# Kernel optimization log

Hardware: AMD Instinct MI355X
Metric: run time of the kernel (lower is better)

Reference implementation:

```python
import jax, jax.numpy as jnp
import numpy as np
from jax import lax

BITS = 8
STRIDE = 1
PADDING = 1
SCALE = 2.0 ** (BITS - 1)  # fixed-point scale 2^(bits-1)


def setup_inputs() -> dict:
    key = jax.random.key(0)
    k1, k2, k3 = jax.random.split(key, 3)
    x = jax.random.normal(k1, (32, 128, 56, 56), dtype=jnp.float32)
    W = jax.random.normal(k2, (256, 128, 3, 3), dtype=jnp.float32)
    b = jax.random.normal(k3, (256,), dtype=jnp.float32)
    return {"x": x, "W": W, "b": b}


def reference(x, W, b):
    # to_fix_point: round(v * 2^(bits-1)); torch keeps long ints, but all
    # arithmetic in forward promotes back to float, so float round is exact here.
    w_q = jnp.round(W * SCALE)
    b_q = jnp.round(b * SCALE)
    # calConv: out[i,j] = sum(patch * w_q) / 2^(bits-1) + b_q
    # (square 3x3 kernel makes the original's transposed patch indexing a standard conv)
    out = lax.conv_general_dilated(
        x, w_q,
        window_strides=(STRIDE, STRIDE),
        padding=[(PADDING, PADDING), (PADDING, PADDING)],
        dimension_numbers=("NCHW", "OIHW", "NCHW"),
    )
    return out / SCALE + b_q[None, :, None, None]
```

## Files before the change

kernel.cpp:

```cpp
#include <hip/hip_runtime.h>

typedef _Float16 half8 __attribute__((ext_vector_type(8)));
typedef float floatx4 __attribute__((ext_vector_type(4)));

#define IMG   3136
#define PIMG  3364
#define XP_ELEMS (32 * 58 * 58 * 128)
#define WQ_ELEMS (9 * 256 * 128)

#define AS1 __attribute__((address_space(1)))
#define AS3 __attribute__((address_space(3)))

__global__ __launch_bounds__(256) void prep_kernel(const float* __restrict__ x,
                                                   const float* __restrict__ W,
                                                   _Float16* __restrict__ xp,
                                                   _Float16* __restrict__ wq) {
    const int bid = blockIdx.x;
    const int t   = threadIdx.x;
    if (bid >= 1856) {
        int U  = (bid - 1856) * 256 + t;
        int l  = U & 63;
        int ni = (U >> 6) & 3;
        int wf = (U >> 8) & 3;
        int s  = U >> 10;
        int rs = s >> 2, cc = s & 3;
        int k  = wf * 64 + ni * 16 + (l & 15);
        int c0 = cc * 32 + (l >> 4) * 8;
        _Float16* d = wq + (long)U * 8;
        #pragma unroll
        for (int j = 0; j < 8; ++j)
            d[j] = (_Float16)rintf(W[(k * 128 + c0 + j) * 9 + rs] * 128.0f);
        return;
    }
    const int hh = bid % 58;
    const int n  = bid / 58;
    _Float16* rowbase = xp + ((long)(n * 58 + hh) * 58) * 128;

    if (hh == 0 || hh == 57) {
        #pragma unroll
        for (int i = 0; i < 4; ++i) {
            int idx = i * 256 + t;
            if (idx < 928) *(half8*)(rowbase + idx * 8) = (half8)(_Float16)0.0f;
        }
        return;
    }

    __shared__ _Float16 tile[128 * 57];
    const int h = hh - 1;

    #pragma unroll
    for (int p = 0; p < 7; ++p) {
        int idx = p * 256 + t;
        int c   = idx / 14;
        int w4  = (idx % 14) * 4;
        const float4 v = *(const float4*)(x + ((long)(n * 128 + c) * 56 + h) * 56 + w4);
        _Float16* d = tile + c * 57 + w4;
        d[0] = (_Float16)v.x; d[1] = (_Float16)v.y;
        d[2] = (_Float16)v.z; d[3] = (_Float16)v.w;
    }
    __syncthreads();

    #pragma unroll
    for (int p = 0; p < 4; ++p) {
        int idx = p * 256 + t;
        if (idx < 896) {
            int ww = idx >> 4;
            int c0 = (idx & 15) * 8;
            half8 v;
            #pragma unroll
            for (int j = 0; j < 8; ++j) v[j] = tile[(c0 + j) * 57 + ww];
            *(half8*)(rowbase + (ww + 1) * 128 + c0) = v;
        }
    }
    if (t < 32) {
        int ww = (t >> 4) ? 57 : 0;
        int c0 = (t & 15) * 8;
        *(half8*)(rowbase + ww * 128 + c0) = (half8)(_Float16)0.0f;
    }
}

__global__ __launch_bounds__(512, 2) void conv_mfma_kernel(
    const _Float16* __restrict__ xp, const _Float16* __restrict__ wq,
    const float* __restrict__ b, float* __restrict__ out)
{
    __shared__ __align__(16) _Float16 smem[16384];

    const int tid = threadIdx.x;
    const int l   = tid & 63;
    const int wv  = tid >> 6;
    const int wp  = wv & 1;
    const int wf  = wv >> 1;
    int bx  = blockIdx.x;
    bx = (bx & 7) * 49 + (bx >> 3);

    long pbB[2];
    #pragma unroll
    for (int h = 0; h < 2; ++h) {
        const int pix = bx * 256 + h * 128 + wv * 16 + (l >> 2);
        const int n = pix / IMG, hw = pix % IMG;
        pbB[h] = (long)(n * PIMG + (hw / 56) * 58 + (hw % 56)) * 256
               + ((l & 3) ^ ((l >> 3) & 3)) * 16;
    }
    const int kq = ((l >> 4) ^ ((l >> 1) & 3)) * 8;

    floatx4 acc[8][4] = {};

    auto stageB = [&](int s, int pbuf) {
        const int rs = s >> 2;
        const int cc = s & 3;
        const int r  = (rs * 11) >> 5;
        const int s2 = rs - r * 3;
        const long toff = (long)(r * 58 + s2) * 256 + cc * 64;
        const char* xb = (const char*)xp + toff;
        _Float16* dst = smem + pbuf * 8192 + wv * 512;
        __builtin_amdgcn_global_load_lds((AS1 void*)(xb + pbB[0]), (AS3 void*)dst,          16, 0, 0);
        __builtin_amdgcn_global_load_lds((AS1 void*)(xb + pbB[1]), (AS3 void*)(dst + 4096), 16, 0, 0);
    };
    auto loadA = [&](int s, half8 (&ff)[4]) {
        const char* base = (const char*)wq + (long)(s * 16 + wf * 4) * 1024 + l * 16;
        #pragma unroll
        for (int ni = 0; ni < 4; ++ni)
            ff[ni] = *(const half8*)(base + ni * 1024);
    };

    auto body = [&](int s, half8 (&ffC)[4], half8 (&ffN)[4]) {
        const int pb = s & 1;
        if (s < 35) {
            loadA(s + 1, ffN);
            stageB(s + 1, pb ^ 1);
            asm volatile("s_waitcnt vmcnt(6)" ::: "memory");
        } else {
            asm volatile("s_waitcnt vmcnt(0)" ::: "memory");
        }
        asm volatile("s_barrier" ::: "memory");
        const _Float16* Bs = smem + pb * 8192;
        __builtin_amdgcn_s_setprio(1);
        #pragma unroll
        for (int mi = 0; mi < 8; ++mi) {
            const half8 pf = *(const half8*)(Bs + (wp * 128 + mi * 16 + (l & 15)) * 32 + kq);
            #pragma unroll
            for (int ni = 0; ni < 4; ++ni)
                acc[mi][ni] = __builtin_amdgcn_mfma_f32_16x16x32_f16(pf, ffC[ni], acc[mi][ni], 0, 0, 0);
        }
        __builtin_amdgcn_s_setprio(0);
        asm volatile("s_barrier" ::: "memory");
    };

    half8 ffA[4], ffB[4];
    loadA(0, ffA);
    stageB(0, 0);
    for (int sp = 0; sp < 18; ++sp) {
        body(2 * sp,     ffA, ffB);
        body(2 * sp + 1, ffB, ffA);
    }

    #pragma unroll
    for (int mi = 0; mi < 8; ++mi) {
        const int pix = bx * 256 + wp * 128 + mi * 16 + (l >> 4) * 4;
        const int n  = pix / IMG;
        const int pr = pix - n * IMG;
        float* orow = out + (long)n * 256 * IMG + pr;
        #pragma unroll
        for (int ni = 0; ni < 4; ++ni) {
            const int filt = wf * 64 + ni * 16 + (l & 15);
            const float bq = rintf(b[filt] * 128.0f);
            float4 v;
            v.x = acc[mi][ni][0] * (1.0f / 128.0f) + bq;
            v.y = acc[mi][ni][1] * (1.0f / 128.0f) + bq;
            v.z = acc[mi][ni][2] * (1.0f / 128.0f) + bq;
            v.w = acc[mi][ni][3] * (1.0f / 128.0f) + bq;
            *(float4*)(orow + (long)filt * IMG) = v;
        }
    }
}

__global__ void conv_fallback_kernel(const float* __restrict__ x, const float* __restrict__ W,
                                     const float* __restrict__ b, float* __restrict__ out)
{
    __shared__ float wsm[1152];
    const int k = blockIdx.y;
    for (int i = threadIdx.x; i < 1152; i += 256)
        wsm[i] = rintf(W[k * 1152 + i] * 128.0f);
    __syncthreads();
    const int pix = blockIdx.x * 256 + threadIdx.x;
    const int n = pix / IMG, hw = pix % IMG;
    const int h = hw / 56, w = hw % 56;
    float acc = 0.0f;
    for (int c = 0; c < 128; ++c) {
        const float* xr = x + ((n * 128 + c) * 56) * 56;
        const float* wr = wsm + c * 9;
        #pragma unroll
        for (int r = 0; r < 3; ++r) {
            const int hh = h + r - 1;
            if ((unsigned)hh >= 56u) continue;
            #pragma unroll
            for (int s = 0; s < 3; ++s) {
                const int ww = w + s - 1;
                if ((unsigned)ww >= 56u) continue;
                acc += xr[hh * 56 + ww] * wr[r * 3 + s];
            }
        }
    }
    out[((long)n * 256 + k) * IMG + hw] = acc * (1.0f / 128.0f) + rintf(b[k] * 128.0f);
}

extern "C" void kernel_launch(void* const* d_in, const int* in_sizes, int n_in,
                              void* d_out, int out_size, void* d_ws, size_t ws_size,
                              hipStream_t stream) {
    const float* x = (const float*)d_in[0];
    const float* W = (const float*)d_in[1];
    const float* b = (const float*)d_in[2];
    float* out = (float*)d_out;

    const size_t need = (size_t)XP_ELEMS * 2 + (size_t)WQ_ELEMS * 2;
    if (ws_size >= need) {
        _Float16* xp = (_Float16*)d_ws;
        _Float16* wq = xp + XP_ELEMS;
        prep_kernel<<<2000, 256, 0, stream>>>(x, W, xp, wq);
        conv_mfma_kernel<<<dim3(392), 512, 0, stream>>>(xp, wq, b, out);
    } else {
        conv_fallback_kernel<<<dim3(392, 256), 256, 0, stream>>>(x, W, b, out);
    }
}
```

Before: 226.5 us.

## Stage weights through LDS with triple-buffered async loads and smaller tiles

The conv kernel now stages both the weight tile and the input patch tile into LDS via global_load_lds, replacing per-wave register loads of weights. The single double buffer becomes a three-deep pipeline, so loads run two stages ahead. Blocks shrink to 256 threads and 128 pixels by all 256 filters, and the grid doubles to 784 blocks. The weight prep layout becomes plain [rs][k][c]. The aim is to hide global latency and raise occupancy, at the cost of more LDS per block and extra LDS reads for the weight fragments.

```diff
diff --git a/kernel.cpp b/kernel.cpp
--- a/kernel.cpp
+++ b/kernel.cpp
@@ -18,18 +18,15 @@
     const int bid = blockIdx.x;
     const int t   = threadIdx.x;
     if (bid >= 1856) {
-        int U  = (bid - 1856) * 256 + t;
-        int l  = U & 63;
-        int ni = (U >> 6) & 3;
-        int wf = (U >> 8) & 3;
-        int s  = U >> 10;
-        int rs = s >> 2, cc = s & 3;
-        int k  = wf * 64 + ni * 16 + (l & 15);
-        int c0 = cc * 32 + (l >> 4) * 8;
-        _Float16* d = wq + (long)U * 8;
-        #pragma unroll
-        for (int j = 0; j < 8; ++j)
-            d[j] = (_Float16)rintf(W[(k * 128 + c0 + j) * 9 + rs] * 128.0f);
+        const long base = ((long)(bid - 1856) * 256 + t) * 8;
+        #pragma unroll
+        for (int j = 0; j < 8; ++j) {
+            const long idx = base + j;
+            const int c  = idx & 127;
+            const int k  = (idx >> 7) & 255;
+            const int rs = idx >> 15;
+            wq[idx] = (_Float16)rintf(W[(k * 128 + c) * 9 + rs] * 128.0f);
+        }
         return;
     }
     const int hh = bid % 58;
@@ -79,90 +76,107 @@
     }
 }
 
-__global__ __launch_bounds__(512, 2) void conv_mfma_kernel(
+__global__ __launch_bounds__(256, 2) void conv_mfma_kernel(
     const _Float16* __restrict__ xp, const _Float16* __restrict__ wq,
     const float* __restrict__ b, float* __restrict__ out)
 {
-    __shared__ __align__(16) _Float16 smem[16384];
+    __shared__ __align__(16) _Float16 smem[36864];
 
     const int tid = threadIdx.x;
     const int l   = tid & 63;
     const int wv  = tid >> 6;
-    const int wp  = wv & 1;
-    const int wf  = wv >> 1;
+    const int wm  = wv & 1;
+    const int wn  = wv >> 1;
     int bx  = blockIdx.x;
-    bx = (bx & 7) * 49 + (bx >> 3);
-
+    bx = (bx & 7) * 98 + (bx >> 3);
+
+    const int lrow = l >> 2;
+    const int lch  = ((l & 3) ^ ((l >> 3) & 3)) * 8;
+    const int kq   = ((l >> 4) ^ ((l >> 1) & 3)) * 8;
+
+    int aoff[4];
+    #pragma unroll
+    for (int i = 0; i < 4; ++i)
+        aoff[i] = (i * 64 + wv * 16 + lrow) * 128 + lch;
     long pbB[2];
     #pragma unroll
-    for (int h = 0; h < 2; ++h) {
-        const int pix = bx * 256 + h * 128 + wv * 16 + (l >> 2);
+    for (int j = 0; j < 2; ++j) {
+        const int pix = bx * 128 + j * 64 + wv * 16 + lrow;
         const int n = pix / IMG, hw = pix % IMG;
-        pbB[h] = (long)(n * PIMG + (hw / 56) * 58 + (hw % 56)) * 256
-               + ((l & 3) ^ ((l >> 3) & 3)) * 16;
-    }
-    const int kq = ((l >> 4) ^ ((l >> 1) & 3)) * 8;
-
-    floatx4 acc[8][4] = {};
-
-    auto stageB = [&](int s, int pbuf) {
+        pbB[j] = (long)(n * PIMG + (hw / 56) * 58 + (hw % 56)) * 128 + lch;
+    }
+    const int stA = wv * 512;
+
+    floatx4 acc[4][8] = {};
+
+    auto stage = [&](int s, int buf) {
         const int rs = s >> 2;
         const int cc = s & 3;
         const int r  = (rs * 11) >> 5;
         const int s2 = rs - r * 3;
-        const long toff = (long)(r * 58 + s2) * 256 + cc * 64;
-        const char* xb = (const char*)xp + toff;
-        _Float16* dst = smem + pbuf * 8192 + wv * 512;
-        __builtin_amdgcn_global_load_lds((AS1 void*)(xb + pbB[0]), (AS3 void*)dst,          16, 0, 0);
-        __builtin_amdgcn_global_load_lds((AS1 void*)(xb + pbB[1]), (AS3 void*)(dst + 4096), 16, 0, 0);
+        const _Float16* wg = wq + rs * (256 * 128) + cc * 32;
+        const _Float16* xg = xp + (r * 58 + s2) * 128 + cc * 32;
+        _Float16* A = smem + buf * 12288 + stA;
+        _Float16* B = smem + buf * 12288 + 8192 + stA;
+        #pragma unroll
+        for (int i = 0; i < 4; ++i)
+            __builtin_amdgcn_global_load_lds((AS1 void*)(wg + aoff[i]),
+                                             (AS3 void*)(A + i * 2048), 16, 0, 0);
+        #pragma unroll
+        for (int j = 0; j < 2; ++j)
+            __builtin_amdgcn_global_load_lds((AS1 void*)(xg + pbB[j]),
+                                             (AS3 void*)(B + j * 2048), 16, 0, 0);
     };
-    auto loadA = [&](int s, half8 (&ff)[4]) {
-        const char* base = (const char*)wq + (long)(s * 16 + wf * 4) * 1024 + l * 16;
-        #pragma unroll
-        for (int ni = 0; ni < 4; ++ni)
-            ff[ni] = *(const half8*)(base + ni * 1024);
-    };
-
-    auto body = [&](int s, half8 (&ffC)[4], half8 (&ffN)[4]) {
-        const int pb = s & 1;
-        if (s < 35) {
-            loadA(s + 1, ffN);
-            stageB(s + 1, pb ^ 1);
+
+    const int frow = wm * 128 + (l & 15);
+    const int prow = wn * 64  + (l & 15);
+
+    stage(0, 0);
+    stage(1, 1);
+
+    #pragma unroll 3
+    for (int s = 0; s < 36; ++s) {
+        const int buf = s % 3;
+        if (s < 34) {
+            stage(s + 2, (s + 2) % 3);
+            asm volatile("s_waitcnt vmcnt(12)" ::: "memory");
+        } else if (s == 34) {
             asm volatile("s_waitcnt vmcnt(6)" ::: "memory");
         } else {
             asm volatile("s_waitcnt vmcnt(0)" ::: "memory");
         }
         asm volatile("s_barrier" ::: "memory");
-        const _Float16* Bs = smem + pb * 8192;
+
+        const _Float16* As = smem + buf * 12288;
+        const _Float16* Bs = As + 8192;
+        half8 pf[4], ff[8];
+        #pragma unroll
+        for (int mi = 0; mi < 4; ++mi)
+            pf[mi] = *(const half8*)(Bs + (prow + mi * 16) * 32 + kq);
+        #pragma unroll
+        for (int ni = 0; ni < 8; ++ni)
+            ff[ni] = *(const half8*)(As + (frow + ni * 16) * 32 + kq);
+
         __builtin_amdgcn_s_setprio(1);
         #pragma unroll
-        for (int mi = 0; mi < 8; ++mi) {
-            const half8 pf = *(const half8*)(Bs + (wp * 128 + mi * 16 + (l & 15)) * 32 + kq);
+        for (int mi = 0; mi < 4; ++mi)
             #pragma unroll
-            for (int ni = 0; ni < 4; ++ni)
-                acc[mi][ni] = __builtin_amdgcn_mfma_f32_16x16x32_f16(pf, ffC[ni], acc[mi][ni], 0, 0, 0);
-        }
+            for (int ni = 0; ni < 8; ++ni)
+                acc[mi][ni] = __builtin_amdgcn_mfma_f32_16x16x32_f16(pf[mi], ff[ni], acc[mi][ni], 0, 0, 0);
         __builtin_amdgcn_s_setprio(0);
+
         asm volatile("s_barrier" ::: "memory");
-    };
-
-    half8 ffA[4], ffB[4];
-    loadA(0, ffA);
-    stageB(0, 0);
-    for (int sp = 0; sp < 18; ++sp) {
-        body(2 * sp,     ffA, ffB);
-        body(2 * sp + 1, ffB, ffA);
-    }
-
-    #pragma unroll
-    for (int mi = 0; mi < 8; ++mi) {
-        const int pix = bx * 256 + wp * 128 + mi * 16 + (l >> 4) * 4;
+    }
+
+    #pragma unroll
+    for (int mi = 0; mi < 4; ++mi) {
+        const int pix = bx * 128 + wn * 64 + mi * 16 + (l >> 4) * 4;
         const int n  = pix / IMG;
         const int pr = pix - n * IMG;
         float* orow = out + (long)n * 256 * IMG + pr;
         #pragma unroll
-        for (int ni = 0; ni < 4; ++ni) {
-            const int filt = wf * 64 + ni * 16 + (l & 15);
+        for (int ni = 0; ni < 8; ++ni) {
+            const int filt = wm * 128 + ni * 16 + (l & 15);
             const float bq = rintf(b[filt] * 128.0f);
             float4 v;
             v.x = acc[mi][ni][0] * (1.0f / 128.0f) + bq;
@@ -217,7 +231,7 @@
         _Float16* xp = (_Float16*)d_ws;
         _Float16* wq = xp + XP_ELEMS;
         prep_kernel<<<2000, 256, 0, stream>>>(x, W, xp, wq);
-        conv_mfma_kernel<<<dim3(392), 512, 0, stream>>>(xp, wq, b, out);
+        conv_mfma_kernel<<<dim3(784), 256, 0, stream>>>(xp, wq, b, out);
     } else {
         conv_fallback_kernel<<<dim3(392, 256), 256, 0, stream>>>(x, W, b, out);
     }
```

After: 213.6 us. 5.7% less time.
